# Performance work log

Measured on AMD Instinct MI355X. Metric: run time of the kernel, lower is better.

## Reference

```python
import jax, jax.numpy as jnp
import numpy as np

B_, S, H, Dh, N = 2, 2048, 8, 64, 32

def setup_inputs() -> dict:
    key = jax.random.key(0)
    k = jax.random.split(key, 6)
    return {
        'u':  jax.random.normal(k[0], (B_, S, H, Dh), dtype=jnp.float32),
        'dt': jax.random.uniform(k[1], (B_, S, H, Dh), dtype=jnp.float32),
        'A':  jax.random.uniform(k[2], (H, Dh, N), dtype=jnp.float32),
        'B':  jax.random.normal(k[3], (B_, S, H, N), dtype=jnp.float32),
        'C':  jax.random.normal(k[4], (B_, S, H, N), dtype=jnp.float32),
        'D':  jax.random.normal(k[5], (H,), dtype=jnp.float32),
    }

def reference(u, dt, A, B, C, D):
    # Selective SSM scan (Mamba-style):
    #   h_t = dA_t * h_{t-1} + dB_t * u_t ; y_t = <h_t, C_t> + D * u_t
    dt_e = dt[..., None]                              # [b,s,h,d,1]
    dA = jnp.exp(-dt_e * A)                           # [b,s,h,d,n]
    Bu = (dt_e * B[:, :, :, None, :]) * u[..., None]  # [b,s,h,d,n]

    def combine(x, y):
        a1, b1 = x
        a2, b2 = y
        return a1 * a2, a2 * b1 + b2

    _, h = jax.lax.associative_scan(combine, (dA, Bu), axis=1)  # inclusive scan over seq
    out = jnp.sum(h * C[:, :, :, None, :], axis=-1)             # [b,s,h,d]
    out = out + D[None, None, :, None] * u
    return out
```

## Files before the change

### kernel.cpp

```cpp
#include <hip/hip_runtime.h>

namespace {

typedef float v2f __attribute__((ext_vector_type(2)));

__device__ __forceinline__ v2f vfma(v2f a, v2f b, v2f c) {
#if __has_builtin(__builtin_elementwise_fma)
    return __builtin_elementwise_fma(a, b, c);
#else
    v2f r; r.x = fmaf(a.x, b.x, c.x); r.y = fmaf(a.y, b.y, c.y); return r;
#endif
}

constexpr int S_LEN = 2048;
constexpr int H_N   = 8;
constexpr int D_DIM = 64;
constexpr int N_DIM = 32;
constexpr int TW    = 32;
constexpr int NKC   = S_LEN / TW;
constexpr int SEGL  = NKC / 4;
constexpr float NLOG2E = -1.4426950408889634f;


__global__ __launch_bounds__(256) void ssm_k1(
    const float* __restrict__ dtp, const float* __restrict__ up,
    const float* __restrict__ Ap,  const float* __restrict__ Bp,
    float* __restrict__ sdtb, float* __restrict__ bagg)
{
    __shared__ float ldt[TW * 64];
    __shared__ float lu [TW * 64];
    __shared__ float lB [TW * 32];

    const int tid  = threadIdx.x;
    const int w    = tid >> 6;
    const int lane = tid & 63;
    const int dl   = lane & 15;
    const int nq   = lane >> 4;
    const int bh   = blockIdx.x >> 6;
    const int kc   = blockIdx.x & 63;
    const int b = bh >> 3, hh = bh & 7;
    const int d  = w * 16 + dl;
    const int n0 = nq * 8;
    const int ch = bh * 64 + d;
    const int s0 = kc * TW;

    const int base_ud = b * (S_LEN * 512) + hh * 64;
    const int bB      = b * (S_LEN * 256) + hh * 32 + s0 * 256;

    {
        const int rB = tid >> 3, cB = tid & 7;
        *(float4*)&lB[rB * 32 + cB * 4] =
            *(const float4*)(Bp + bB + rB * 256 + cB * 4);
#pragma unroll
        for (int it = 0; it < 2; ++it) {
            const int idx = it * 256 + tid;
            const int r = idx >> 4, c = idx & 15;
            const int g = base_ud + (s0 + r) * 512 + c * 4;
            *(float4*)&ldt[r * 64 + c * 4] = *(const float4*)(dtp + g);
            *(float4*)&lu [r * 64 + c * 4] = *(const float4*)(up  + g);
        }
    }

    v2f Aneg2[4];
    {
        const float* Arow = Ap + (hh * D_DIM + d) * N_DIM + n0;
#pragma unroll
        for (int j = 0; j < 4; ++j) {
            v2f a2 = *(const v2f*)(Arow + 2 * j);
            Aneg2[j] = a2 * NLOG2E;
        }
    }

    __syncthreads();

    v2f bA2[4];
#pragma unroll
    for (int j = 0; j < 4; ++j) bA2[j] = (v2f)(0.0f);
    float sdt = 0.0f;

#pragma unroll 4
    for (int tt = 0; tt < TW; ++tt) {
        const float dtv = ldt[tt * 64 + d];
        const float uv  = lu [tt * 64 + d];
        const float kk  = dtv * uv;
        sdt += dtv;
        const v2f dt2 = (v2f)(dtv);
        const v2f kk2 = (v2f)(kk);
#pragma unroll
        for (int j = 0; j < 4; ++j) {
            const v2f B2 = *(const v2f*)&lB[tt * 32 + n0 + 2 * j];
            const v2f arg = dt2 * Aneg2[j];
            v2f e;
            e.x = __builtin_amdgcn_exp2f(arg.x);
            e.y = __builtin_amdgcn_exp2f(arg.y);
            bA2[j] = vfma(e, bA2[j], kk2 * B2);
        }
    }

    if (nq == 0) sdtb[kc * 1024 + ch] = sdt;
    {
        float* dst = bagg + (size_t)kc * 32768 + ch * 32 + n0;
        *(float4*)(dst + 0) = make_float4(bA2[0].x, bA2[0].y, bA2[1].x, bA2[1].y);
        *(float4*)(dst + 4) = make_float4(bA2[2].x, bA2[2].y, bA2[3].x, bA2[3].y);
    }
}

__global__ __launch_bounds__(256) void ssm_k2(
    const float* __restrict__ sdtb, const float* __restrict__ bagg,
    const float* __restrict__ Ap,   float* __restrict__ pref)
{
    const int T   = blockIdx.x * 256 + threadIdx.x;
    const int seg = T & 3;
    const int n   = (T >> 2) & 31;
    const int ch  = T >> 7;
    const int d   = ch & 63;
    const int hh  = (ch >> 6) & 7;
    const float Aneg1 = NLOG2E * Ap[(hh * D_DIM + d) * N_DIM + n];

    const int k0 = seg * SEGL;
    const size_t base = (size_t)ch * 32 + n;

    float bb[SEGL], av[SEGL];
#pragma unroll
    for (int i = 0; i < SEGL; ++i) {
        bb[i] = bagg[(size_t)(k0 + i) * 32768 + base];
        av[i] = sdtb[(k0 + i) * 1024 + ch];
    }
#pragma unroll
    for (int i = 0; i < SEGL; ++i)
        av[i] = __builtin_amdgcn_exp2f(Aneg1 * av[i]);

    float bseg = 0.0f, Aseg = 1.0f;
#pragma unroll
    for (int i = 0; i < SEGL; ++i) {
        bseg = fmaf(av[i], bseg, bb[i]);
        Aseg *= av[i];
    }

    {
        float Au = __shfl_up(Aseg, 1, 4), bu = __shfl_up(bseg, 1, 4);
        if (seg >= 1) { bseg = fmaf(Aseg, bu, bseg); Aseg *= Au; }
        Au = __shfl_up(Aseg, 2, 4); bu = __shfl_up(bseg, 2, 4);
        if (seg >= 2) { bseg = fmaf(Aseg, bu, bseg); Aseg *= Au; }
    }
    const float ebu = __shfl_up(bseg, 1, 4);
    float p = (seg == 0) ? 0.0f : ebu;

#pragma unroll
    for (int i = 0; i < SEGL; ++i) {
        pref[(size_t)(k0 + i) * 32768 + base] = p;
        p = fmaf(av[i], p, bb[i]);
    }
}

__global__ __launch_bounds__(256) void ssm_k3(
    const float* __restrict__ dtp, const float* __restrict__ up,
    const float* __restrict__ Ap,  const float* __restrict__ Bp,
    const float* __restrict__ Cp,  const float* __restrict__ Dp,
    const float* __restrict__ pref, float* __restrict__ outp)
{
    __shared__ float ldt[TW * 64];
    __shared__ float lu [TW * 64];
    __shared__ float lB [TW * 32];
    __shared__ float lC [TW * 32];

    const int tid  = threadIdx.x;
    const int w    = tid >> 6;
    const int lane = tid & 63;
    const int dl   = lane & 15;
    const int nq   = lane >> 4;
    const int bh   = blockIdx.x >> 6;
    const int kc   = blockIdx.x & 63;
    const int b = bh >> 3, hh = bh & 7;
    const int d  = w * 16 + dl;
    const int n0 = nq * 8;
    const int ch = bh * 64 + d;
    const int s0 = kc * TW;

    const int base_ud = b * (S_LEN * 512) + hh * 64;
    const int bB      = b * (S_LEN * 256) + hh * 32 + s0 * 256;

    {
        const int rB = tid >> 3, cB = tid & 7;
        *(float4*)&lB[rB * 32 + cB * 4] =
            *(const float4*)(Bp + bB + rB * 256 + cB * 4);
        *(float4*)&lC[rB * 32 + cB * 4] =
            *(const float4*)(Cp + bB + rB * 256 + cB * 4);
#pragma unroll
        for (int it = 0; it < 2; ++it) {
            const int idx = it * 256 + tid;
            const int r = idx >> 4, c = idx & 15;
            const int g = base_ud + (s0 + r) * 512 + c * 4;
            *(float4*)&ldt[r * 64 + c * 4] = *(const float4*)(dtp + g);
            *(float4*)&lu [r * 64 + c * 4] = *(const float4*)(up  + g);
        }
    }

    v2f h2[4];
    {
        const float* ps = pref + (size_t)kc * 32768 + ch * 32 + n0;
        float4 v0 = *(const float4*)(ps + 0);
        float4 v1 = *(const float4*)(ps + 4);
        h2[0].x = v0.x; h2[0].y = v0.y; h2[1].x = v0.z; h2[1].y = v0.w;
        h2[2].x = v1.x; h2[2].y = v1.y; h2[3].x = v1.z; h2[3].y = v1.w;
    }

    v2f Aneg2[4];
    {
        const float* Arow = Ap + (hh * D_DIM + d) * N_DIM + n0;
#pragma unroll
        for (int j = 0; j < 4; ++j) {
            v2f a2 = *(const v2f*)(Arow + 2 * j);
            Aneg2[j] = a2 * NLOG2E;
        }
    }

    const float Dv = Dp[hh];

    __syncthreads();

#pragma unroll 4
    for (int tt = 0; tt < TW; ++tt) {
        const float dtv = ldt[tt * 64 + d];
        const float uv  = lu [tt * 64 + d];
        const float kk  = dtv * uv;
        const v2f dt2 = (v2f)(dtv);
        const v2f kk2 = (v2f)(kk);
        v2f ya = (v2f)(0.0f);
        v2f yb = (v2f)(0.0f);
#pragma unroll
        for (int j = 0; j < 4; ++j) {
            const v2f B2 = *(const v2f*)&lB[tt * 32 + n0 + 2 * j];
            const v2f C2 = *(const v2f*)&lC[tt * 32 + n0 + 2 * j];
            const v2f arg = dt2 * Aneg2[j];
            v2f e;
            e.x = __builtin_amdgcn_exp2f(arg.x);
            e.y = __builtin_amdgcn_exp2f(arg.y);
            h2[j] = vfma(e, h2[j], kk2 * B2);
            if (j & 1) yb = vfma(h2[j], C2, yb);
            else       ya = vfma(h2[j], C2, ya);
        }
        float y = (ya.x + ya.y) + (yb.x + yb.y);
        y += __shfl_xor(y, 16);
        y += __shfl_xor(y, 32);
        if (nq == 0) outp[base_ud + d + (s0 + tt) * 512] = fmaf(Dv, uv, y);
    }
}

}

extern "C" void kernel_launch(void* const* d_in, const int* in_sizes, int n_in,
                              void* d_out, int out_size, void* d_ws, size_t ws_size,
                              hipStream_t stream)
{
    const float* u  = (const float*)d_in[0];
    const float* dt = (const float*)d_in[1];
    const float* A  = (const float*)d_in[2];
    const float* B  = (const float*)d_in[3];
    const float* C  = (const float*)d_in[4];
    const float* D  = (const float*)d_in[5];
    float* out = (float*)d_out;

    float* sdtb = (float*)d_ws;
    float* bagg = sdtb + (size_t)NKC * 1024;
    float* pref = bagg + (size_t)NKC * 32 * 1024;

    ssm_k1<<<dim3(16 * NKC), dim3(256), 0, stream>>>(dt, u, A, B, sdtb, bagg);
    ssm_k2<<<dim3(512),      dim3(256), 0, stream>>>(sdtb, bagg, A, pref);
    ssm_k3<<<dim3(16 * NKC), dim3(256), 0, stream>>>(dt, u, A, B, C, D, pref, out);
}
```

Before: 41.71 us.

## Split chunk staging into two halves to overlap global loads with compute

The k1 and k3 kernels now stage the 32-step chunk in two 16-step halves. The second half's global loads are issued into registers before the first half is computed, then written to a separate shared buffer. This hides part of the global-load latency behind the first half's exp/FMA work instead of stalling on the full chunk up front. It costs extra registers for the in-flight float4 values, and with few timesteps per block the overlap window is small.

```diff
diff --git a/kernel.cpp b/kernel.cpp
--- a/kernel.cpp
+++ b/kernel.cpp
@@ -17,6 +17,7 @@
 constexpr int D_DIM = 64;
 constexpr int N_DIM = 32;
 constexpr int TW    = 32;
+constexpr int HALF  = 16;
 constexpr int NKC   = S_LEN / TW;
 constexpr int SEGL  = NKC / 4;
 constexpr float NLOG2E = -1.4426950408889634f;
@@ -27,9 +28,9 @@
     const float* __restrict__ Ap,  const float* __restrict__ Bp,
     float* __restrict__ sdtb, float* __restrict__ bagg)
 {
-    __shared__ float ldt[TW * 64];
-    __shared__ float lu [TW * 64];
-    __shared__ float lB [TW * 32];
+    __shared__ float ldt[2][HALF * 64];
+    __shared__ float lu [2][HALF * 64];
+    __shared__ float lB [2][HALF * 32];
 
     const int tid  = threadIdx.x;
     const int w    = tid >> 6;
@@ -47,19 +48,13 @@
     const int base_ud = b * (S_LEN * 512) + hh * 64;
     const int bB      = b * (S_LEN * 256) + hh * 32 + s0 * 256;
 
-    {
-        const int rB = tid >> 3, cB = tid & 7;
-        *(float4*)&lB[rB * 32 + cB * 4] =
-            *(const float4*)(Bp + bB + rB * 256 + cB * 4);
-#pragma unroll
-        for (int it = 0; it < 2; ++it) {
-            const int idx = it * 256 + tid;
-            const int r = idx >> 4, c = idx & 15;
-            const int g = base_ud + (s0 + r) * 512 + c * 4;
-            *(float4*)&ldt[r * 64 + c * 4] = *(const float4*)(dtp + g);
-            *(float4*)&lu [r * 64 + c * 4] = *(const float4*)(up  + g);
-        }
-    }
+    const int rT = tid >> 4, cT = tid & 15;
+    const int rB8 = tid >> 3, cB8 = tid & 7;
+
+    float4 rdt = *(const float4*)(dtp + base_ud + (s0 + rT) * 512 + cT * 4);
+    float4 ru  = *(const float4*)(up  + base_ud + (s0 + rT) * 512 + cT * 4);
+    float4 rb;
+    if (tid < 128) rb = *(const float4*)(Bp + bB + rB8 * 256 + cB8 * 4);
 
     v2f Aneg2[4];
     {
@@ -71,31 +66,49 @@
         }
     }
 
-    __syncthreads();
+    *(float4*)&ldt[0][rT * 64 + cT * 4] = rdt;
+    *(float4*)&lu [0][rT * 64 + cT * 4] = ru;
+    if (tid < 128) *(float4*)&lB[0][rB8 * 32 + cB8 * 4] = rb;
+    __syncthreads();
+
+    rdt = *(const float4*)(dtp + base_ud + (s0 + HALF + rT) * 512 + cT * 4);
+    ru  = *(const float4*)(up  + base_ud + (s0 + HALF + rT) * 512 + cT * 4);
+    if (tid < 128) rb = *(const float4*)(Bp + bB + HALF * 256 + rB8 * 256 + cB8 * 4);
 
     v2f bA2[4];
 #pragma unroll
     for (int j = 0; j < 4; ++j) bA2[j] = (v2f)(0.0f);
     float sdt = 0.0f;
 
+    auto compute_half = [&](int hf) {
 #pragma unroll 4
-    for (int tt = 0; tt < TW; ++tt) {
-        const float dtv = ldt[tt * 64 + d];
-        const float uv  = lu [tt * 64 + d];
-        const float kk  = dtv * uv;
-        sdt += dtv;
-        const v2f dt2 = (v2f)(dtv);
-        const v2f kk2 = (v2f)(kk);
-#pragma unroll
-        for (int j = 0; j < 4; ++j) {
-            const v2f B2 = *(const v2f*)&lB[tt * 32 + n0 + 2 * j];
-            const v2f arg = dt2 * Aneg2[j];
-            v2f e;
-            e.x = __builtin_amdgcn_exp2f(arg.x);
-            e.y = __builtin_amdgcn_exp2f(arg.y);
-            bA2[j] = vfma(e, bA2[j], kk2 * B2);
-        }
-    }
+        for (int t2 = 0; t2 < HALF; ++t2) {
+            const float dtv = ldt[hf][t2 * 64 + d];
+            const float uv  = lu [hf][t2 * 64 + d];
+            const float kk  = dtv * uv;
+            sdt += dtv;
+            const v2f dt2 = (v2f)(dtv);
+            const v2f kk2 = (v2f)(kk);
+#pragma unroll
+            for (int j = 0; j < 4; ++j) {
+                const v2f B2 = *(const v2f*)&lB[hf][t2 * 32 + n0 + 2 * j];
+                const v2f arg = dt2 * Aneg2[j];
+                v2f e;
+                e.x = __builtin_amdgcn_exp2f(arg.x);
+                e.y = __builtin_amdgcn_exp2f(arg.y);
+                bA2[j] = vfma(e, bA2[j], kk2 * B2);
+            }
+        }
+    };
+
+    compute_half(0);
+
+    *(float4*)&ldt[1][rT * 64 + cT * 4] = rdt;
+    *(float4*)&lu [1][rT * 64 + cT * 4] = ru;
+    if (tid < 128) *(float4*)&lB[1][rB8 * 32 + cB8 * 4] = rb;
+    __syncthreads();
+
+    compute_half(1);
 
     if (nq == 0) sdtb[kc * 1024 + ch] = sdt;
     {
@@ -159,10 +172,10 @@
     const float* __restrict__ Cp,  const float* __restrict__ Dp,
     const float* __restrict__ pref, float* __restrict__ outp)
 {
-    __shared__ float ldt[TW * 64];
-    __shared__ float lu [TW * 64];
-    __shared__ float lB [TW * 32];
-    __shared__ float lC [TW * 32];
+    __shared__ float ldt[2][HALF * 64];
+    __shared__ float lu [2][HALF * 64];
+    __shared__ float lB [2][HALF * 32];
+    __shared__ float lC [2][HALF * 32];
 
     const int tid  = threadIdx.x;
     const int w    = tid >> 6;
@@ -180,21 +193,15 @@
     const int base_ud = b * (S_LEN * 512) + hh * 64;
     const int bB      = b * (S_LEN * 256) + hh * 32 + s0 * 256;
 
-    {
-        const int rB = tid >> 3, cB = tid & 7;
-        *(float4*)&lB[rB * 32 + cB * 4] =
-            *(const float4*)(Bp + bB + rB * 256 + cB * 4);
-        *(float4*)&lC[rB * 32 + cB * 4] =
-            *(const float4*)(Cp + bB + rB * 256 + cB * 4);
-#pragma unroll
-        for (int it = 0; it < 2; ++it) {
-            const int idx = it * 256 + tid;
-            const int r = idx >> 4, c = idx & 15;
-            const int g = base_ud + (s0 + r) * 512 + c * 4;
-            *(float4*)&ldt[r * 64 + c * 4] = *(const float4*)(dtp + g);
-            *(float4*)&lu [r * 64 + c * 4] = *(const float4*)(up  + g);
-        }
-    }
+    const int rT = tid >> 4, cT = tid & 15;
+    const int t8 = tid & 127;
+    const int rB8 = t8 >> 3, cB8 = t8 & 7;
+
+    float4 rdt = *(const float4*)(dtp + base_ud + (s0 + rT) * 512 + cT * 4);
+    float4 ru  = *(const float4*)(up  + base_ud + (s0 + rT) * 512 + cT * 4);
+    float4 rbc;
+    if (tid < 128) rbc = *(const float4*)(Bp + bB + rB8 * 256 + cB8 * 4);
+    else           rbc = *(const float4*)(Cp + bB + rB8 * 256 + cB8 * 4);
 
     v2f h2[4];
     {
@@ -204,7 +211,6 @@
         h2[0].x = v0.x; h2[0].y = v0.y; h2[1].x = v0.z; h2[1].y = v0.w;
         h2[2].x = v1.x; h2[2].y = v1.y; h2[3].x = v1.z; h2[3].y = v1.w;
     }
-
     v2f Aneg2[4];
     {
         const float* Arow = Ap + (hh * D_DIM + d) * N_DIM + n0;
@@ -214,37 +220,58 @@
             Aneg2[j] = a2 * NLOG2E;
         }
     }
-
     const float Dv = Dp[hh];
 
-    __syncthreads();
-
+    *(float4*)&ldt[0][rT * 64 + cT * 4] = rdt;
+    *(float4*)&lu [0][rT * 64 + cT * 4] = ru;
+    if (tid < 128) *(float4*)&lB[0][rB8 * 32 + cB8 * 4] = rbc;
+    else           *(float4*)&lC[0][rB8 * 32 + cB8 * 4] = rbc;
+    __syncthreads();
+
+    rdt = *(const float4*)(dtp + base_ud + (s0 + HALF + rT) * 512 + cT * 4);
+    ru  = *(const float4*)(up  + base_ud + (s0 + HALF + rT) * 512 + cT * 4);
+    if (tid < 128) rbc = *(const float4*)(Bp + bB + HALF * 256 + rB8 * 256 + cB8 * 4);
+    else           rbc = *(const float4*)(Cp + bB + HALF * 256 + rB8 * 256 + cB8 * 4);
+
+    auto compute_half = [&](int hf) {
 #pragma unroll 4
-    for (int tt = 0; tt < TW; ++tt) {
-        const float dtv = ldt[tt * 64 + d];
-        const float uv  = lu [tt * 64 + d];
-        const float kk  = dtv * uv;
-        const v2f dt2 = (v2f)(dtv);
-        const v2f kk2 = (v2f)(kk);
-        v2f ya = (v2f)(0.0f);
-        v2f yb = (v2f)(0.0f);
-#pragma unroll
-        for (int j = 0; j < 4; ++j) {
-            const v2f B2 = *(const v2f*)&lB[tt * 32 + n0 + 2 * j];
-            const v2f C2 = *(const v2f*)&lC[tt * 32 + n0 + 2 * j];
-            const v2f arg = dt2 * Aneg2[j];
-            v2f e;
-            e.x = __builtin_amdgcn_exp2f(arg.x);
-            e.y = __builtin_amdgcn_exp2f(arg.y);
-            h2[j] = vfma(e, h2[j], kk2 * B2);
-            if (j & 1) yb = vfma(h2[j], C2, yb);
-            else       ya = vfma(h2[j], C2, ya);
-        }
-        float y = (ya.x + ya.y) + (yb.x + yb.y);
-        y += __shfl_xor(y, 16);
-        y += __shfl_xor(y, 32);
-        if (nq == 0) outp[base_ud + d + (s0 + tt) * 512] = fmaf(Dv, uv, y);
-    }
+        for (int t2 = 0; t2 < HALF; ++t2) {
+            const float dtv = ldt[hf][t2 * 64 + d];
+            const float uv  = lu [hf][t2 * 64 + d];
+            const float kk  = dtv * uv;
+            const v2f dt2 = (v2f)(dtv);
+            const v2f kk2 = (v2f)(kk);
+            v2f ya = (v2f)(0.0f);
+            v2f yb = (v2f)(0.0f);
+#pragma unroll
+            for (int j = 0; j < 4; ++j) {
+                const v2f B2 = *(const v2f*)&lB[hf][t2 * 32 + n0 + 2 * j];
+                const v2f C2 = *(const v2f*)&lC[hf][t2 * 32 + n0 + 2 * j];
+                const v2f arg = dt2 * Aneg2[j];
+                v2f e;
+                e.x = __builtin_amdgcn_exp2f(arg.x);
+                e.y = __builtin_amdgcn_exp2f(arg.y);
+                h2[j] = vfma(e, h2[j], kk2 * B2);
+                if (j & 1) yb = vfma(h2[j], C2, yb);
+                else       ya = vfma(h2[j], C2, ya);
+            }
+            float y = (ya.x + ya.y) + (yb.x + yb.y);
+            y += __shfl_xor(y, 16);
+            y += __shfl_xor(y, 32);
+            if (nq == 0)
+                outp[base_ud + d + (s0 + hf * HALF + t2) * 512] = fmaf(Dv, uv, y);
+        }
+    };
+
+    compute_half(0);
+
+    *(float4*)&ldt[1][rT * 64 + cT * 4] = rdt;
+    *(float4*)&lu [1][rT * 64 + cT * 4] = ru;
+    if (tid < 128) *(float4*)&lB[1][rB8 * 32 + cB8 * 4] = rbc;
+    else           *(float4*)&lC[1][rB8 * 32 + cB8 * 4] = rbc;
+    __syncthreads();
+
+    compute_half(1);
 }
 
 }
```

After: 41.50 us. Within noise of the previous version (-0.5%).
